# Performance work log

Hardware: AMD Instinct MI355X
Metric: run time of the kernel (lower is better)

The kernel has to match this reference:

```python
import jax, jax.numpy as jnp
import numpy as np

N_HEADS = 16  # matches init_kwargs

def setup_inputs() -> dict:
    key = jax.random.key(0)
    ks = jax.random.split(key, 7)
    B, S, D = 2, 2048, 2048
    return {
        "query": jax.random.normal(ks[0], (B, S, D), jnp.float32),
        "key":   jax.random.normal(ks[1], (B, S, D), jnp.float32),
        "value": jax.random.normal(ks[2], (B, S, D), jnp.float32),
        "Wq": jax.random.normal(ks[3], (D, D), jnp.float32) * 0.02,
        "Wk": jax.random.normal(ks[4], (D, D), jnp.float32) * 0.02,
        "Wv": jax.random.normal(ks[5], (D, D), jnp.float32) * 0.02,
        "Wo": jax.random.normal(ks[6], (D, D), jnp.float32) * 0.02,
        "block_size": 64,
    }

def reference(query, key, value, Wq, Wk, Wv, Wo, block_size):
    # Faithful to the torch module: softmax is applied INDEPENDENTLY per
    # k-block (no online-softmax rescaling) and block outputs are summed.
    B, S, D = query.shape
    H = N_HEADS
    hd = D // H
    nb = S // block_size  # number of k-blocks (S is a multiple of block_size)
    scale = jnp.asarray(np.sqrt(hd), query.dtype)

    # nn.Linear(bias=False): y = x @ W.T
    q = (query @ Wq.T).reshape(B, S, H, hd).transpose(0, 2, 1, 3)  # [B,H,S,hd]
    k = (key   @ Wk.T).reshape(B, S, H, hd).transpose(0, 2, 1, 3)
    v = (value @ Wv.T).reshape(B, S, H, hd).transpose(0, 2, 1, 3)

    kb = k.reshape(B, H, nb, block_size, hd)  # k-blocks
    vb = v.reshape(B, H, nb, block_size, hd)

    scores = jnp.einsum('bhsd,bhnkd->bhsnk', q, kb) / scale  # [B,H,S,nb,bs]
    attn = jax.nn.softmax(scores, axis=-1)  # per-block softmax (as in source)
    out = jnp.einsum('bhsnk,bhnkd->bhsd', attn, vb)  # sum over blocks

    attn_weights = attn.reshape(B, H, S, S)  # full materialized attn matrix
    out = out.transpose(0, 2, 1, 3).reshape(B, S, D) @ Wo.T
    return out, attn_weights
```

## Files before the change

### kernel.cpp

```cpp
#include <hip/hip_runtime.h>

typedef unsigned short u16;
typedef unsigned int u32;
typedef __attribute__((ext_vector_type(8))) __bf16 bf16x8;
typedef __attribute__((ext_vector_type(4))) float f32x4;

__device__ __forceinline__ void gl_lds16(const void* g, void* l) {
  __builtin_amdgcn_global_load_lds((__attribute__((address_space(1))) void*)g,
                                   (__attribute__((address_space(3))) void*)l,
                                   16, 0, 0);
}

__device__ __forceinline__ u16 f2bf(float f) {
  u32 x = __builtin_bit_cast(u32, f);
  return (u16)((x + 0x7fffu + ((x >> 16) & 1u)) >> 16);
}

__global__ __launch_bounds__(256) void cvt_bf16(const float* __restrict__ in,
                                                u16* __restrict__ out, int n) {
  int i = (blockIdx.x * 256 + threadIdx.x) * 8;
  if (i >= n) return;
  const float4* p = (const float4*)(in + i);
  float4 a = p[0], b = p[1];
  uint4 u;
  u.x = f2bf(a.x) | ((u32)f2bf(a.y) << 16);
  u.y = f2bf(a.z) | ((u32)f2bf(a.w) << 16);
  u.z = f2bf(b.x) | ((u32)f2bf(b.y) << 16);
  u.w = f2bf(b.z) | ((u32)f2bf(b.w) << 16);
  *(uint4*)(out + i) = u;
}

__global__ __launch_bounds__(256) void transpose_2048(const u16* __restrict__ in,
                                                      u16* __restrict__ out) {
  __shared__ u16 tile[32][33];
  const size_t base = (size_t)blockIdx.z * 2048 * 2048;
  int x = blockIdx.x * 32 + threadIdx.x;
  int y = blockIdx.y * 32 + threadIdx.y;
  for (int j = 0; j < 32; j += 8)
    tile[threadIdx.y + j][threadIdx.x] = in[base + (size_t)(y + j) * 2048 + x];
  __syncthreads();
  x = blockIdx.y * 32 + threadIdx.x;
  y = blockIdx.x * 32 + threadIdx.y;
  for (int j = 0; j < 32; j += 8)
    out[base + (size_t)(y + j) * 2048 + x] = tile[threadIdx.x][threadIdx.y + j];
}

template <bool F32OUT>
__global__ __launch_bounds__(256, 2)
void gemm_bt(const u16* __restrict__ A, const u16* __restrict__ B,
             void* __restrict__ Cptr, int M, int N, int K) {
  __shared__ u16 As[128 * 32];
  __shared__ u16 Bs[128 * 32];
  const int tid = threadIdx.x;
  const int lane = tid & 63, w = tid >> 6;
  const int m0 = blockIdx.y * 128, n0 = blockIdx.x * 128;
  const int wm = (w & 1) * 64, wn = (w >> 1) * 64;
  const int fm = lane & 15, quad = lane >> 4;
  const int sr = lane >> 2, sc = lane & 3;
  f32x4 acc[4][4] = {};
  for (int k0 = 0; k0 < K; k0 += 32) {
    __syncthreads();
    for (int i = w; i < 8; i += 4) {
      int r = i * 16 + sr;
      int ca = sc ^ ((r >> 1) & 3);
      gl_lds16(A + (size_t)(m0 + r) * K + k0 + ca * 8, &As[i * 512]);
      gl_lds16(B + (size_t)(n0 + r) * K + k0 + ca * 8, &Bs[i * 512]);
    }
    __syncthreads();
    bf16x8 af[4], bfr[4];
#pragma unroll
    for (int t = 0; t < 4; t++) {
      int ra = wm + t * 16 + fm;
      af[t] = *(const bf16x8*)&As[ra * 32 + ((quad ^ ((ra >> 1) & 3)) << 3)];
      int rb = wn + t * 16 + fm;
      bfr[t] = *(const bf16x8*)&Bs[rb * 32 + ((quad ^ ((rb >> 1) & 3)) << 3)];
    }
#pragma unroll
    for (int mt = 0; mt < 4; mt++)
#pragma unroll
      for (int nt = 0; nt < 4; nt++)
        acc[mt][nt] = __builtin_amdgcn_mfma_f32_16x16x32_bf16(af[mt], bfr[nt], acc[mt][nt], 0, 0, 0);
  }
  const int er = quad * 4;
#pragma unroll
  for (int mt = 0; mt < 4; mt++)
#pragma unroll
    for (int nt = 0; nt < 4; nt++)
#pragma unroll
      for (int r = 0; r < 4; r++) {
        size_t idx = (size_t)(m0 + wm + mt * 16 + er + r) * N + (n0 + wn + nt * 16 + fm);
        if (F32OUT) ((float*)Cptr)[idx] = acc[mt][nt][r];
        else        ((u16*)Cptr)[idx] = f2bf(acc[mt][nt][r]);
      }
}

__global__ __launch_bounds__(256, 2)
void attn_kernel(const u16* __restrict__ Q, const u16* __restrict__ Kmat,
                 const u16* __restrict__ Vt, float* __restrict__ attn_out,
                 u16* __restrict__ ctx) {
  __shared__ u16 Ks[64 * 128];
  __shared__ u16 Vts[128 * 64];
  __shared__ u16 Ps[128 * 64];
  const int tid = threadIdx.x, lane = tid & 63, w = tid >> 6;
  const int qt = blockIdx.x, h = blockIdx.y, b = blockIdx.z;
  const int q0 = qt * 128;
  const int fm = lane & 15, quad = lane >> 4;
  const float inv_scale = 0.08838834764831845f;

  bf16x8 qf[2][4];
  {
    const u16* Qg = Q + (size_t)(b * 2048 + q0 + w * 32 + fm) * 2048 + h * 128;
#pragma unroll
    for (int mt = 0; mt < 2; mt++)
#pragma unroll
      for (int kt = 0; kt < 4; kt++)
        qf[mt][kt] = *(const bf16x8*)(Qg + (size_t)mt * 16 * 2048 + kt * 32 + quad * 8);
  }
  f32x4 cacc[2][8] = {};
  const u16* Kg = Kmat + (size_t)b * 2048 * 2048 + h * 128;
  const u16* Vg = Vt + (size_t)(b * 16 + h) * 128 * 2048;
  const int krl = lane >> 4, kcl = lane & 15;
  const int vrl = lane >> 3, vcl = lane & 7;

  for (int kb = 0; kb < 32; kb++) {
    __syncthreads();
    for (int i = w; i < 16; i += 4) {
      int rk = i * 4 + krl;
      int ck = kcl ^ (rk & 15);
      gl_lds16(Kg + (size_t)(kb * 64 + rk) * 2048 + ck * 8, &Ks[i * 512]);
      int rv = i * 8 + vrl;
      int cv = vcl ^ (rv & 7);
      gl_lds16(Vg + (size_t)rv * 2048 + kb * 64 + cv * 8, &Vts[i * 512]);
    }
    __syncthreads();

    f32x4 sacc[2][4] = {};
#pragma unroll
    for (int kt = 0; kt < 4; kt++) {
      bf16x8 kf[4];
#pragma unroll
      for (int nt = 0; nt < 4; nt++) {
        int rk = nt * 16 + fm;
        int ck = (kt * 4 + quad) ^ (rk & 15);
        kf[nt] = *(const bf16x8*)&Ks[rk * 128 + ck * 8];
      }
#pragma unroll
      for (int mt = 0; mt < 2; mt++)
#pragma unroll
        for (int nt = 0; nt < 4; nt++)
          sacc[mt][nt] = __builtin_amdgcn_mfma_f32_16x16x32_bf16(qf[mt][kt], kf[nt], sacc[mt][nt], 0, 0, 0);
    }

#pragma unroll
    for (int mt = 0; mt < 2; mt++)
#pragma unroll
      for (int r = 0; r < 4; r++) {
        float v0 = sacc[mt][0][r], v1 = sacc[mt][1][r], v2 = sacc[mt][2][r], v3 = sacc[mt][3][r];
        float mx = fmaxf(fmaxf(v0, v1), fmaxf(v2, v3));
        mx = fmaxf(mx, __shfl_xor(mx, 1));
        mx = fmaxf(mx, __shfl_xor(mx, 2));
        mx = fmaxf(mx, __shfl_xor(mx, 4));
        mx = fmaxf(mx, __shfl_xor(mx, 8));
        float e0 = __expf((v0 - mx) * inv_scale);
        float e1 = __expf((v1 - mx) * inv_scale);
        float e2 = __expf((v2 - mx) * inv_scale);
        float e3 = __expf((v3 - mx) * inv_scale);
        float s = e0 + e1 + e2 + e3;
        s += __shfl_xor(s, 1);
        s += __shfl_xor(s, 2);
        s += __shfl_xor(s, 4);
        s += __shfl_xor(s, 8);
        float inv = 1.0f / s;
        float p0 = e0 * inv, p1 = e1 * inv, p2 = e2 * inv, p3 = e3 * inv;
        int row = w * 32 + mt * 16 + quad * 4 + r;
        size_t ob = ((size_t)((b * 16 + h) * 2048 + q0 + row)) * 2048 + kb * 64;
        attn_out[ob + fm] = p0;
        attn_out[ob + 16 + fm] = p1;
        attn_out[ob + 32 + fm] = p2;
        attn_out[ob + 48 + fm] = p3;
        int rw7 = row & 7, fh = fm >> 3, fl = fm & 7;
        u16* pp = &Ps[row * 64];
        pp[(((0 + fh) ^ rw7) << 3) + fl] = f2bf(p0);
        pp[(((2 + fh) ^ rw7) << 3) + fl] = f2bf(p1);
        pp[(((4 + fh) ^ rw7) << 3) + fl] = f2bf(p2);
        pp[(((6 + fh) ^ rw7) << 3) + fl] = f2bf(p3);
      }

#pragma unroll
    for (int kt = 0; kt < 2; kt++) {
      bf16x8 pa[2], vb[8];
#pragma unroll
      for (int mt = 0; mt < 2; mt++) {
        int rp = w * 32 + mt * 16 + fm;
        int cp = (kt * 4 + quad) ^ (rp & 7);
        pa[mt] = *(const bf16x8*)&Ps[rp * 64 + cp * 8];
      }
#pragma unroll
      for (int nt = 0; nt < 8; nt++) {
        int rv = nt * 16 + fm;
        int cv = (kt * 4 + quad) ^ (rv & 7);
        vb[nt] = *(const bf16x8*)&Vts[rv * 64 + cv * 8];
      }
#pragma unroll
      for (int mt = 0; mt < 2; mt++)
#pragma unroll
        for (int nt = 0; nt < 8; nt++)
          cacc[mt][nt] = __builtin_amdgcn_mfma_f32_16x16x32_bf16(pa[mt], vb[nt], cacc[mt][nt], 0, 0, 0);
    }
  }

#pragma unroll
  for (int mt = 0; mt < 2; mt++)
#pragma unroll
    for (int nt = 0; nt < 8; nt++)
#pragma unroll
      for (int r = 0; r < 4; r++) {
        int row = q0 + w * 32 + mt * 16 + quad * 4 + r;
        int col = h * 128 + nt * 16 + fm;
        ctx[(size_t)(b * 2048 + row) * 2048 + col] = f2bf(cacc[mt][nt][r]);
      }
}

extern "C" void kernel_launch(void* const* d_in, const int* in_sizes, int n_in,
                              void* d_out, int out_size, void* d_ws, size_t ws_size,
                              hipStream_t stream) {
  const float* query = (const float*)d_in[0];
  const float* key   = (const float*)d_in[1];
  const float* value = (const float*)d_in[2];
  const float* Wq = (const float*)d_in[3];
  const float* Wk = (const float*)d_in[4];
  const float* Wv = (const float*)d_in[5];
  const float* Wo = (const float*)d_in[6];

  float* out  = (float*)d_out;
  float* attn = out + (size_t)8388608;

  u16* ws  = (u16*)d_ws;
  u16* wqb = ws;
  u16* wkb = wqb + 4194304;
  u16* wvb = wkb + 4194304;
  u16* wob = wvb + 4194304;
  u16* Qb  = wob + 4194304;
  u16* Kb  = Qb + 8388608;
  u16* Vb  = Kb + 8388608;
  u16* Vtb = Vb + 8388608;
  u16* ctx = Vtb + 8388608;
  u16* Xq = (u16*)attn;
  u16* Xk = Xq + 8388608;
  u16* Xv = Xk + 8388608;

  cvt_bf16<<<4096, 256, 0, stream>>>(query, Xq, 8388608);
  cvt_bf16<<<4096, 256, 0, stream>>>(key,   Xk, 8388608);
  cvt_bf16<<<4096, 256, 0, stream>>>(value, Xv, 8388608);
  cvt_bf16<<<2048, 256, 0, stream>>>(Wq, wqb, 4194304);
  cvt_bf16<<<2048, 256, 0, stream>>>(Wk, wkb, 4194304);
  cvt_bf16<<<2048, 256, 0, stream>>>(Wv, wvb, 4194304);
  cvt_bf16<<<2048, 256, 0, stream>>>(Wo, wob, 4194304);

  dim3 gg(16, 32, 1);
  gemm_bt<false><<<gg, 256, 0, stream>>>(Xq, wqb, Qb, 4096, 2048, 2048);
  gemm_bt<false><<<gg, 256, 0, stream>>>(Xk, wkb, Kb, 4096, 2048, 2048);
  gemm_bt<false><<<gg, 256, 0, stream>>>(Xv, wvb, Vb, 4096, 2048, 2048);

  transpose_2048<<<dim3(64, 64, 2), dim3(32, 8), 0, stream>>>(Vb, Vtb);

  attn_kernel<<<dim3(16, 16, 2), 256, 0, stream>>>(Qb, Kb, Vtb, attn, ctx);

  gemm_bt<true><<<gg, 256, 0, stream>>>(ctx, wob, out, 4096, 2048, 2048);
}
```

Baseline: 1.031 ms.

## Fuse conversions and QKV GEMMs, compute V transposed, double-buffer attention loads

```diff
diff --git a/kernel.cpp b/kernel.cpp
--- a/kernel.cpp
+++ b/kernel.cpp
@@ -16,44 +16,46 @@
   return (u16)((x + 0x7fffu + ((x >> 16) & 1u)) >> 16);
 }
 
-__global__ __launch_bounds__(256) void cvt_bf16(const float* __restrict__ in,
-                                                u16* __restrict__ out, int n) {
-  int i = (blockIdx.x * 256 + threadIdx.x) * 8;
-  if (i >= n) return;
-  const float4* p = (const float4*)(in + i);
+__global__ __launch_bounds__(256) void cvt_all(
+    const float* __restrict__ q, const float* __restrict__ k, const float* __restrict__ v,
+    const float* __restrict__ wq, const float* __restrict__ wk, const float* __restrict__ wv,
+    const float* __restrict__ wo,
+    u16* __restrict__ xq, u16* __restrict__ xk, u16* __restrict__ xv,
+    u16* __restrict__ owq, u16* __restrict__ owk, u16* __restrict__ owv,
+    u16* __restrict__ owo) {
+  int bid = blockIdx.x;
+  const float* src;
+  u16* dst;
+  int chunk;
+  if (bid < 12288) {
+    int t = bid >> 12;
+    chunk = bid & 4095;
+    src = (t == 0) ? q : (t == 1) ? k : v;
+    dst = (t == 0) ? xq : (t == 1) ? xk : xv;
+  } else {
+    int b2 = bid - 12288;
+    int t = b2 >> 11;
+    chunk = b2 & 2047;
+    src = (t == 0) ? wq : (t == 1) ? wk : (t == 2) ? wv : wo;
+    dst = (t == 0) ? owq : (t == 1) ? owk : (t == 2) ? owv : owo;
+  }
+  int i = (chunk * 256 + (int)threadIdx.x) * 8;
+  const float4* p = (const float4*)(src + i);
   float4 a = p[0], b = p[1];
   uint4 u;
   u.x = f2bf(a.x) | ((u32)f2bf(a.y) << 16);
   u.y = f2bf(a.z) | ((u32)f2bf(a.w) << 16);
   u.z = f2bf(b.x) | ((u32)f2bf(b.y) << 16);
   u.w = f2bf(b.z) | ((u32)f2bf(b.w) << 16);
-  *(uint4*)(out + i) = u;
-}
-
-__global__ __launch_bounds__(256) void transpose_2048(const u16* __restrict__ in,
-                                                      u16* __restrict__ out) {
-  __shared__ u16 tile[32][33];
-  const size_t base = (size_t)blockIdx.z * 2048 * 2048;
-  int x = blockIdx.x * 32 + threadIdx.x;
-  int y = blockIdx.y * 32 + threadIdx.y;
-  for (int j = 0; j < 32; j += 8)
-    tile[threadIdx.y + j][threadIdx.x] = in[base + (size_t)(y + j) * 2048 + x];
-  __syncthreads();
-  x = blockIdx.y * 32 + threadIdx.x;
-  y = blockIdx.x * 32 + threadIdx.y;
-  for (int j = 0; j < 32; j += 8)
-    out[base + (size_t)(y + j) * 2048 + x] = tile[threadIdx.x][threadIdx.y + j];
+  *(uint4*)(dst + i) = u;
 }
 
 template <bool F32OUT>
-__global__ __launch_bounds__(256, 2)
-void gemm_bt(const u16* __restrict__ A, const u16* __restrict__ B,
-             void* __restrict__ Cptr, int M, int N, int K) {
-  __shared__ u16 As[128 * 32];
-  __shared__ u16 Bs[128 * 32];
+__device__ __forceinline__ void gemm_body(const u16* __restrict__ A, const u16* __restrict__ B,
+                                          void* __restrict__ Cptr, int m0, int n0, int N, int K,
+                                          u16* As, u16* Bs) {
   const int tid = threadIdx.x;
   const int lane = tid & 63, w = tid >> 6;
-  const int m0 = blockIdx.y * 128, n0 = blockIdx.x * 128;
   const int wm = (w & 1) * 64, wn = (w >> 1) * 64;
   const int fm = lane & 15, quad = lane >> 4;
   const int sr = lane >> 2, sc = lane & 3;
@@ -95,17 +97,47 @@
 }
 
 __global__ __launch_bounds__(256, 2)
+void gemm_qkv(const u16* __restrict__ Xq, const u16* __restrict__ Wqb, u16* __restrict__ Qb,
+              const u16* __restrict__ Xk, const u16* __restrict__ Wkb, u16* __restrict__ Kb,
+              const u16* __restrict__ Xv, const u16* __restrict__ Wvb, u16* __restrict__ Vt) {
+  __shared__ u16 As[128 * 32];
+  __shared__ u16 Bs[128 * 32];
+  const int bid = blockIdx.x, z = blockIdx.y;
+  const u16 *A, *B;
+  u16* C;
+  int N, m0, n0;
+  if (z == 0) {
+    A = Xq; B = Wqb; C = Qb; N = 2048;
+    m0 = (bid >> 4) << 7; n0 = (bid & 15) << 7;
+  } else if (z == 1) {
+    A = Xk; B = Wkb; C = Kb; N = 2048;
+    m0 = (bid >> 4) << 7; n0 = (bid & 15) << 7;
+  } else {
+    A = Wvb; B = Xv; C = Vt; N = 4096;
+    m0 = (bid >> 5) << 7; n0 = (bid & 31) << 7;
+  }
+  gemm_body<false>(A, B, C, m0, n0, N, 2048, As, Bs);
+}
+
+__global__ __launch_bounds__(256, 2)
+void gemm_out(const u16* __restrict__ A, const u16* __restrict__ B, float* __restrict__ C) {
+  __shared__ u16 As[128 * 32];
+  __shared__ u16 Bs[128 * 32];
+  gemm_body<true>(A, B, C, (int)(blockIdx.y << 7), (int)(blockIdx.x << 7), 2048, 2048, As, Bs);
+}
+
+__global__ __launch_bounds__(256, 2)
 void attn_kernel(const u16* __restrict__ Q, const u16* __restrict__ Kmat,
                  const u16* __restrict__ Vt, float* __restrict__ attn_out,
                  u16* __restrict__ ctx) {
-  __shared__ u16 Ks[64 * 128];
-  __shared__ u16 Vts[128 * 64];
+  __shared__ u16 Ks[2][64 * 128];
+  __shared__ u16 Vts[2][128 * 64];
   __shared__ u16 Ps[128 * 64];
   const int tid = threadIdx.x, lane = tid & 63, w = tid >> 6;
   const int qt = blockIdx.x, h = blockIdx.y, b = blockIdx.z;
   const int q0 = qt * 128;
   const int fm = lane & 15, quad = lane >> 4;
-  const float inv_scale = 0.08838834764831845f;
+  const float c_e2 = 0.088388347648318447f * 1.4426950408889634f;
 
   bf16x8 qf[2][4];
   {
@@ -118,21 +150,27 @@
   }
   f32x4 cacc[2][8] = {};
   const u16* Kg = Kmat + (size_t)b * 2048 * 2048 + h * 128;
-  const u16* Vg = Vt + (size_t)(b * 16 + h) * 128 * 2048;
+  const u16* Vg = Vt + (size_t)(h * 128) * 4096 + b * 2048;
   const int krl = lane >> 4, kcl = lane & 15;
   const int vrl = lane >> 3, vcl = lane & 7;
 
+#define STAGE(buf, kbb)                                                              \
+  for (int i = w; i < 16; i += 4) {                                                  \
+    int rk = i * 4 + krl;                                                            \
+    int ck = kcl ^ (rk & 15);                                                        \
+    gl_lds16(Kg + (size_t)((kbb) * 64 + rk) * 2048 + ck * 8, &Ks[(buf)][i * 512]);   \
+    int rv = i * 8 + vrl;                                                            \
+    int cv = vcl ^ (rv & 7);                                                         \
+    gl_lds16(Vg + (size_t)rv * 4096 + (kbb) * 64 + cv * 8, &Vts[(buf)][i * 512]);    \
+  }
+
+  STAGE(0, 0)
+  asm volatile("s_waitcnt vmcnt(0)" ::: "memory");
+  __builtin_amdgcn_s_barrier();
+
   for (int kb = 0; kb < 32; kb++) {
-    __syncthreads();
-    for (int i = w; i < 16; i += 4) {
-      int rk = i * 4 + krl;
-      int ck = kcl ^ (rk & 15);
-      gl_lds16(Kg + (size_t)(kb * 64 + rk) * 2048 + ck * 8, &Ks[i * 512]);
-      int rv = i * 8 + vrl;
-      int cv = vcl ^ (rv & 7);
-      gl_lds16(Vg + (size_t)rv * 2048 + kb * 64 + cv * 8, &Vts[i * 512]);
-    }
-    __syncthreads();
+    const int cur = kb & 1;
+    if (kb < 31) { STAGE(cur ^ 1, kb + 1) }
 
     f32x4 sacc[2][4] = {};
 #pragma unroll
@@ -142,13 +180,15 @@
       for (int nt = 0; nt < 4; nt++) {
         int rk = nt * 16 + fm;
         int ck = (kt * 4 + quad) ^ (rk & 15);
-        kf[nt] = *(const bf16x8*)&Ks[rk * 128 + ck * 8];
-      }
+        kf[nt] = *(const bf16x8*)&Ks[cur][rk * 128 + ck * 8];
+      }
+      __builtin_amdgcn_s_setprio(1);
 #pragma unroll
       for (int mt = 0; mt < 2; mt++)
 #pragma unroll
         for (int nt = 0; nt < 4; nt++)
           sacc[mt][nt] = __builtin_amdgcn_mfma_f32_16x16x32_bf16(qf[mt][kt], kf[nt], sacc[mt][nt], 0, 0, 0);
+      __builtin_amdgcn_s_setprio(0);
     }
 
 #pragma unroll
@@ -161,16 +201,16 @@
         mx = fmaxf(mx, __shfl_xor(mx, 2));
         mx = fmaxf(mx, __shfl_xor(mx, 4));
         mx = fmaxf(mx, __shfl_xor(mx, 8));
-        float e0 = __expf((v0 - mx) * inv_scale);
-        float e1 = __expf((v1 - mx) * inv_scale);
-        float e2 = __expf((v2 - mx) * inv_scale);
-        float e3 = __expf((v3 - mx) * inv_scale);
+        float e0 = exp2f((v0 - mx) * c_e2);
+        float e1 = exp2f((v1 - mx) * c_e2);
+        float e2 = exp2f((v2 - mx) * c_e2);
+        float e3 = exp2f((v3 - mx) * c_e2);
         float s = e0 + e1 + e2 + e3;
         s += __shfl_xor(s, 1);
         s += __shfl_xor(s, 2);
         s += __shfl_xor(s, 4);
         s += __shfl_xor(s, 8);
-        float inv = 1.0f / s;
+        float inv = __builtin_amdgcn_rcpf(s);
         float p0 = e0 * inv, p1 = e1 * inv, p2 = e2 * inv, p3 = e3 * inv;
         int row = w * 32 + mt * 16 + quad * 4 + r;
         size_t ob = ((size_t)((b * 16 + h) * 2048 + q0 + row)) * 2048 + kb * 64;
@@ -199,15 +239,23 @@
       for (int nt = 0; nt < 8; nt++) {
         int rv = nt * 16 + fm;
         int cv = (kt * 4 + quad) ^ (rv & 7);
-        vb[nt] = *(const bf16x8*)&Vts[rv * 64 + cv * 8];
-      }
+        vb[nt] = *(const bf16x8*)&Vts[cur][rv * 64 + cv * 8];
+      }
+      __builtin_amdgcn_s_setprio(1);
 #pragma unroll
       for (int mt = 0; mt < 2; mt++)
 #pragma unroll
         for (int nt = 0; nt < 8; nt++)
           cacc[mt][nt] = __builtin_amdgcn_mfma_f32_16x16x32_bf16(pa[mt], vb[nt], cacc[mt][nt], 0, 0, 0);
-    }
-  }
+      __builtin_amdgcn_s_setprio(0);
+    }
+
+    if (kb < 31) {
+      asm volatile("s_waitcnt vmcnt(0)" ::: "memory");
+      __builtin_amdgcn_s_barrier();
+    }
+  }
+#undef STAGE
 
 #pragma unroll
   for (int mt = 0; mt < 2; mt++)
@@ -242,29 +290,18 @@
   u16* wob = wvb + 4194304;
   u16* Qb  = wob + 4194304;
   u16* Kb  = Qb + 8388608;
-  u16* Vb  = Kb + 8388608;
-  u16* Vtb = Vb + 8388608;
+  u16* Vtb = Kb + 8388608;
   u16* ctx = Vtb + 8388608;
   u16* Xq = (u16*)attn;
   u16* Xk = Xq + 8388608;
   u16* Xv = Xk + 8388608;
 
-  cvt_bf16<<<4096, 256, 0, stream>>>(query, Xq, 8388608);
-  cvt_bf16<<<4096, 256, 0, stream>>>(key,   Xk, 8388608);
-  cvt_bf16<<<4096, 256, 0, stream>>>(value, Xv, 8388608);
-  cvt_bf16<<<2048, 256, 0, stream>>>(Wq, wqb, 4194304);
-  cvt_bf16<<<2048, 256, 0, stream>>>(Wk, wkb, 4194304);
-  cvt_bf16<<<2048, 256, 0, stream>>>(Wv, wvb, 4194304);
-  cvt_bf16<<<2048, 256, 0, stream>>>(Wo, wob, 4194304);
-
-  dim3 gg(16, 32, 1);
-  gemm_bt<false><<<gg, 256, 0, stream>>>(Xq, wqb, Qb, 4096, 2048, 2048);
-  gemm_bt<false><<<gg, 256, 0, stream>>>(Xk, wkb, Kb, 4096, 2048, 2048);
-  gemm_bt<false><<<gg, 256, 0, stream>>>(Xv, wvb, Vb, 4096, 2048, 2048);
-
-  transpose_2048<<<dim3(64, 64, 2), dim3(32, 8), 0, stream>>>(Vb, Vtb);
+  cvt_all<<<20480, 256, 0, stream>>>(query, key, value, Wq, Wk, Wv, Wo,
+                                     Xq, Xk, Xv, wqb, wkb, wvb, wob);
+
+  gemm_qkv<<<dim3(512, 3, 1), 256, 0, stream>>>(Xq, wqb, Qb, Xk, wkb, Kb, Xv, wvb, Vtb);
 
   attn_kernel<<<dim3(16, 16, 2), 256, 0, stream>>>(Qb, Kb, Vtb, attn, ctx);
 
-  gemm_bt<true><<<gg, 256, 0, stream>>>(ctx, wob, out, 4096, 2048, 2048);
-}
+  gemm_out<<<dim3(16, 32, 1), 256, 0, stream>>>(ctx, wob, out);
+}
```

Measured after the change: 996.5 us. 3.3% less time.
